# Performance work log

Hardware: AMD Instinct MI355X
Metric: run time of the kernel (lower is better)

Reference implementation:

```python
import jax, jax.numpy as jnp
import numpy as np

N1, N2, E, D, DOUT = 20000, 20000, 1000000, 64, 64


def setup_inputs() -> dict:
    key = jax.random.key(0)
    ks = jax.random.split(key, 10)
    node1 = jax.random.normal(ks[0], (N1, D), jnp.float32)
    node2 = jax.random.normal(ks[1], (N2, D), jnp.float32)
    seg_i1 = jax.random.randint(ks[2], (E,), 0, N1, dtype=jnp.int32)
    idx_j1 = jax.random.randint(ks[3], (E,), 0, 64, dtype=jnp.int32)
    seg_i2 = jax.random.randint(ks[4], (E,), 0, N2, dtype=jnp.int32)
    idx_j2 = jax.random.randint(ks[5], (E,), 0, 64, dtype=jnp.int32)
    xav = float(np.sqrt(2.0 / (D + D)))  # xavier_normal for square proj
    Wk = jax.random.normal(ks[6], (D, D), jnp.float32) * xav
    Wv = jax.random.normal(ks[7], (D, D), jnp.float32) * xav
    Wo = jax.random.normal(ks[8], (D, DOUT), jnp.float32) * float(np.sqrt(1.0 / D))
    bo = jnp.zeros((DOUT,), jnp.float32)
    return {"node1": node1, "seg_i1": seg_i1, "idx_j1": idx_j1,
            "node2": node2, "seg_i2": seg_i2, "idx_j2": idx_j2,
            "Wk": Wk, "Wv": Wv, "Wo": Wo, "bo": bo}


def _segment_softmax(logit, seg, n_seg, temperature):
    # faithful to torch segment_softmax: max is detached; idx_j dense-buffer
    # trick is equivalent to a true segment max for unique (seg, idx) pairs
    m = jax.lax.stop_gradient(jax.ops.segment_max(logit, seg, num_segments=n_seg))
    e = jnp.exp((logit - m[seg]) / temperature)
    s = jax.ops.segment_sum(e, seg, num_segments=n_seg)
    return e / (s[seg] + 1e-8)


def reference(node1, seg_i1, idx_j1, node2, seg_i2, idx_j2, Wk, Wv, Wo, bo):
    d_h = node1.shape[1]
    n_seg1, n_seg2 = node1.shape[0], node2.shape[0]
    temperature = float(np.sqrt(d_h))

    node1_ctr = (node1 @ Wk)[seg_i1]   # [E, d_h]
    node2_ctr = (node2 @ Wk)[seg_i2]
    node1_nbr = (node2 @ Wv)[seg_i2]
    node2_nbr = (node1 @ Wv)[seg_i1]

    translation = jnp.sum(node1_ctr * node2_ctr, axis=1)  # [E]

    node1_edge = _segment_softmax(translation, seg_i1, n_seg1, temperature)
    node2_edge = _segment_softmax(translation, seg_i2, n_seg2, temperature)

    msg1 = jax.ops.segment_sum(node1_edge[:, None] * node1_nbr, seg_i1, num_segments=n_seg1)
    msg2 = jax.ops.segment_sum(node2_edge[:, None] * node2_nbr, seg_i2, num_segments=n_seg2)

    msg1 = jax.nn.leaky_relu(msg1 @ Wo + bo, negative_slope=0.01)
    msg2 = jax.nn.leaky_relu(msg2 @ Wo + bo, negative_slope=0.01)
    return msg1, msg2, node1_edge[:, None], node2_edge[:, None]
```

## Files before the change

kernel.cpp:

```cpp
#include <hip/hip_runtime.h>
#include <math.h>

#define BSH 7
#define BSZ (1 << BSH)
#define MAXNB 256
#define PT_TILE 4096

typedef __attribute__((ext_vector_type(4))) float f32x4;
typedef __attribute__((ext_vector_type(8))) short bf16x8;

__device__ __forceinline__ float readlane_f(float v, int l) {
    return __uint_as_float((unsigned)__builtin_amdgcn_readlane((int)__float_as_uint(v), l));
}
__device__ __forceinline__ unsigned short f2b(float f) {
    unsigned u = __float_as_uint(f);
    return (unsigned short)((u + 0x7FFFu + ((u >> 16) & 1u)) >> 16);
}
__device__ __forceinline__ float blo(unsigned u) { return __uint_as_float(u << 16); }
__device__ __forceinline__ float bhi(unsigned u) { return __uint_as_float(u & 0xFFFF0000u); }

__global__ void proj_kernel(const float* __restrict__ X1, int n1,
                            const float* __restrict__ X2, int n2,
                            const float* __restrict__ Wk,
                            const float* __restrict__ Wv,
                            unsigned short* __restrict__ K1, unsigned short* __restrict__ V1,
                            unsigned short* __restrict__ K2, unsigned short* __restrict__ V2,
                            int* bcnt1, int* bcnt2, int nb1, int nb2) {
    __shared__ float sWk[64 * 64];
    __shared__ float sWv[64 * 64];
    int tid = threadIdx.x;
    if (blockIdx.x == 0) {
        for (int i = tid; i < nb1; i += blockDim.x) bcnt1[i] = 0;
        for (int i = tid; i < nb2; i += blockDim.x) bcnt2[i] = 0;
    }
    for (int i = tid; i < 1024; i += blockDim.x) {
        ((float4*)sWk)[i] = ((const float4*)Wk)[i];
        ((float4*)sWv)[i] = ((const float4*)Wv)[i];
    }
    __syncthreads();
    int wave = tid >> 6, lane = tid & 63;
    int wpb = blockDim.x >> 6;
    int total = n1 + n2;
    for (int idx = blockIdx.x * wpb + wave; idx < total; idx += gridDim.x * wpb) {
        const float* X; unsigned short* K; unsigned short* V; long r;
        if (idx < n1) { X = X1; K = K1; V = V1; r = idx; }
        else { X = X2; K = K2; V = V2; r = idx - n1; }
        float x = X[r * 64 + lane];
        float ak = 0.f, av = 0.f;
#pragma unroll
        for (int k = 0; k < 64; ++k) {
            float xv = __shfl(x, k);
            ak = fmaf(xv, sWk[k * 64 + lane], ak);
            av = fmaf(xv, sWv[k * 64 + lane], av);
        }
        K[r * 64 + lane] = f2b(ak);
        V[r * 64 + lane] = f2b(av);
    }
}

__global__ void logit_kernel(const unsigned short* __restrict__ K1,
                             const unsigned short* __restrict__ K2,
                             const int* __restrict__ seg1, const int* __restrict__ seg2,
                             float* __restrict__ trans, int E) {
    int tid = blockIdx.x * blockDim.x + threadIdx.x;
    int e = tid >> 3, g = tid & 7;
    if (e >= E) return;
    int i1 = seg1[e], i2 = seg2[e];
    uint4 a = *(const uint4*)(K1 + (long)i1 * 64 + g * 8);
    uint4 b = *(const uint4*)(K2 + (long)i2 * 64 + g * 8);
    float d = blo(a.x) * blo(b.x);
    d = fmaf(bhi(a.x), bhi(b.x), d);
    d = fmaf(blo(a.y), blo(b.y), d);
    d = fmaf(bhi(a.y), bhi(b.y), d);
    d = fmaf(blo(a.z), blo(b.z), d);
    d = fmaf(bhi(a.z), bhi(b.z), d);
    d = fmaf(blo(a.w), blo(b.w), d);
    d = fmaf(bhi(a.w), bhi(b.w), d);
    d += __shfl_xor(d, 1);
    d += __shfl_xor(d, 2);
    d += __shfl_xor(d, 4);
    if (g == 0) trans[e] = d;
}

__global__ void bucket_count_kernel(const int* __restrict__ seg1, const int* __restrict__ seg2,
                                    int E, int* bcnt1, int* bcnt2, int nb1, int nb2) {
    __shared__ int c1[MAXNB], c2[MAXNB];
    int tid = threadIdx.x;
    for (int i = tid; i < MAXNB; i += blockDim.x) { c1[i] = 0; c2[i] = 0; }
    __syncthreads();
    for (int i = blockIdx.x * blockDim.x + tid; i < E; i += gridDim.x * blockDim.x) {
        atomicAdd(&c1[seg1[i] >> BSH], 1);
        atomicAdd(&c2[seg2[i] >> BSH], 1);
    }
    __syncthreads();
    for (int i = tid; i < nb1; i += blockDim.x) if (c1[i]) atomicAdd(&bcnt1[i], c1[i]);
    for (int i = tid; i < nb2; i += blockDim.x) if (c2[i]) atomicAdd(&bcnt2[i], c2[i]);
}

__global__ void bucket_scan_kernel(const int* __restrict__ bcnt1, const int* __restrict__ bcnt2,
                                   int* bb1, int* bb2, int* bcur1, int* bcur2,
                                   int nb1, int nb2, int E) {
    __shared__ int tmp[MAXNB];
    int t = threadIdx.x;
    int v1 = (t < nb1) ? bcnt1[t] : 0;
    tmp[t] = v1;
    __syncthreads();
    for (int off = 1; off < MAXNB; off <<= 1) {
        int x = (t >= off) ? tmp[t - off] : 0;
        __syncthreads();
        tmp[t] += x;
        __syncthreads();
    }
    if (t < nb1) { int excl = tmp[t] - v1; bb1[t] = excl; bcur1[t] = excl; }
    if (t == 0) bb1[nb1] = E;
    __syncthreads();
    int v2 = (t < nb2) ? bcnt2[t] : 0;
    tmp[t] = v2;
    __syncthreads();
    for (int off = 1; off < MAXNB; off <<= 1) {
        int x = (t >= off) ? tmp[t - off] : 0;
        __syncthreads();
        tmp[t] += x;
        __syncthreads();
    }
    if (t < nb2) { int excl = tmp[t] - v2; bb2[t] = excl; bcur2[t] = excl; }
    if (t == 0) bb2[nb2] = E;
}

__global__ void partition_kernel(const int* __restrict__ seg1, const int* __restrict__ seg2,
                                 const float* __restrict__ trans, int E,
                                 int* bcur1, int* bcur2,
                                 float2* __restrict__ tmp1, float2* __restrict__ tmp2) {
    __shared__ int c1[MAXNB], c2[MAXNB];
    int tid = threadIdx.x;
    int base = blockIdx.x * PT_TILE;
    int end = base + PT_TILE;
    if (end > E) end = E;
    for (int i = tid; i < MAXNB; i += blockDim.x) { c1[i] = 0; c2[i] = 0; }
    __syncthreads();
    for (int i = base + tid; i < end; i += blockDim.x) {
        atomicAdd(&c1[seg1[i] >> BSH], 1);
        atomicAdd(&c2[seg2[i] >> BSH], 1);
    }
    __syncthreads();
    for (int i = tid; i < MAXNB; i += blockDim.x) {
        int n = c1[i]; c1[i] = n ? atomicAdd(&bcur1[i], n) : 0;
        n = c2[i];     c2[i] = n ? atomicAdd(&bcur2[i], n) : 0;
    }
    __syncthreads();
    for (int i = base + tid; i < end; i += blockDim.x) {
        int s1 = seg1[i], s2 = seg2[i];
        float t = trans[i];
        int p = atomicAdd(&c1[s1 >> BSH], 1);
        tmp1[p] = make_float2(t, __int_as_float(((s1 & (BSZ - 1)) << 25) | s2));
        int q = atomicAdd(&c2[s2 >> BSH], 1);
        tmp2[q] = make_float2(t, __int_as_float(((s2 & (BSZ - 1)) << 25) | s1));
    }
}

__global__ void bin2_kernel(const float2* __restrict__ tmp1, const int* __restrict__ bb1,
                            int n1, int* __restrict__ cur1, int* __restrict__ deg1,
                            float2* __restrict__ csr1,
                            const float2* __restrict__ tmp2, const int* __restrict__ bb2,
                            int n2, int* __restrict__ cur2, int* __restrict__ deg2,
                            float2* __restrict__ csr2, int nb1) {
    __shared__ int cnt[BSZ];
    __shared__ int off[BSZ];
    __shared__ int sc[BSZ];
    int b = blockIdx.x;
    const float2* tmp; const int* bb; int n; int* cur; int* deg; float2* csr;
    if (b < nb1) { tmp = tmp1; bb = bb1; n = n1; cur = cur1; deg = deg1; csr = csr1; }
    else { b -= nb1; tmp = tmp2; bb = bb2; n = n2; cur = cur2; deg = deg2; csr = csr2; }
    int tid = threadIdx.x;
    int node0 = b << BSH;
    int s = bb[b], e_end = bb[b + 1];
    for (int i = tid; i < BSZ; i += blockDim.x) cnt[i] = 0;
    __syncthreads();
    for (int i = s + tid; i < e_end; i += blockDim.x)
        atomicAdd(&cnt[((unsigned)__float_as_int(tmp[i].y)) >> 25], 1);
    __syncthreads();
    if (tid < BSZ) sc[tid] = cnt[tid];
    __syncthreads();
    for (int o = 1; o < BSZ; o <<= 1) {
        int x = (tid >= o && tid < BSZ) ? sc[tid - o] : 0;
        __syncthreads();
        if (tid < BSZ) sc[tid] += x;
        __syncthreads();
    }
    if (tid < BSZ) {
        int excl = sc[tid] - cnt[tid] + s;
        off[tid] = excl;
        int node = node0 + tid;
        if (node < n) { cur[node] = excl; deg[node] = cnt[tid]; }
    }
    __syncthreads();
    for (int i = s + tid; i < e_end; i += blockDim.x) {
        float2 r = tmp[i];
        unsigned pay = (unsigned)__float_as_int(r.y);
        int pos = atomicAdd(&off[pay >> 25], 1);
        csr[pos] = make_float2(r.x, __int_as_float((int)(pay & 0x1FFFFFFu)));
    }
}

__global__ void gather_ms_kernel(int n1, int n2,
                                 const int* __restrict__ cur1, const int* __restrict__ deg1,
                                 const float2* __restrict__ csr1,
                                 const unsigned short* __restrict__ Vb2,
                                 float2* __restrict__ minv1,
                                 const int* __restrict__ cur2, const int* __restrict__ deg2,
                                 const float2* __restrict__ csr2,
                                 const unsigned short* __restrict__ Vb1,
                                 float2* __restrict__ minv2,
                                 unsigned short* __restrict__ msgr,
                                 float invT) {
    int tid = threadIdx.x;
    int wave = tid >> 6, lane = tid & 63;
    int wpb = blockDim.x >> 6;
    int g = lane >> 4, l = lane & 15;
    int total = n1 + n2;
    for (int idx = blockIdx.x * wpb + wave; idx < total; idx += gridDim.x * wpb) {
        const int *cur, *deg; const float2* csr; const unsigned short* V;
        float2* minv; int nd;
        if (idx < n1) {
            cur = cur1; deg = deg1; csr = csr1; V = Vb2; minv = minv1; nd = idx;
        } else {
            cur = cur2; deg = deg2; csr = csr2; V = Vb1; minv = minv2; nd = idx - n1;
        }
        int d = deg[nd];
        int start = cur[nd];
        float4 acc = make_float4(0.f, 0.f, 0.f, 0.f);
        if (d > 0) {
            float t0 = -INFINITY, t1 = -INFINITY, t2 = -INFINITY;
            int j0 = 0, j1 = 0, j2 = 0;
            if (lane < d)       { float2 r = csr[start + lane];       t0 = r.x; j0 = __float_as_int(r.y); }
            if (lane + 64 < d)  { float2 r = csr[start + lane + 64];  t1 = r.x; j1 = __float_as_int(r.y); }
            if (lane + 128 < d) { float2 r = csr[start + lane + 128]; t2 = r.x; j2 = __float_as_int(r.y); }
            float m = fmaxf(fmaxf(t0, t1), t2);
            for (int k = 192 + lane; k < d; k += 64) m = fmaxf(m, csr[start + k].x);
            m = fmaxf(m, __shfl_xor(m, 1));
            m = fmaxf(m, __shfl_xor(m, 2));
            m = fmaxf(m, __shfl_xor(m, 4));
            m = fmaxf(m, __shfl_xor(m, 8));
            m = fmaxf(m, __shfl_xor(m, 16));
            m = fmaxf(m, __shfl_xor(m, 32));
            float p0 = (lane < d)       ? __expf((t0 - m) * invT) : 0.f;
            float p1 = (lane + 64 < d)  ? __expf((t1 - m) * invT) : 0.f;
            float p2 = (lane + 128 < d) ? __expf((t2 - m) * invT) : 0.f;
            float s = p0 + p1 + p2;
            for (int k = 192 + lane; k < d; k += 64) s += __expf((csr[start + k].x - m) * invT);
            s += __shfl_xor(s, 1);
            s += __shfl_xor(s, 2);
            s += __shfl_xor(s, 4);
            s += __shfl_xor(s, 8);
            s += __shfl_xor(s, 16);
            s += __shfl_xor(s, 32);
            float inv = 1.f / (s + 1e-8f);
            if (lane == 0) minv[nd] = make_float2(m, inv);
            unsigned u0 = ((unsigned)f2b(p0 * inv) << 16) | (unsigned)j0;
            unsigned u1 = ((unsigned)f2b(p1 * inv) << 16) | (unsigned)j1;
            unsigned u2 = ((unsigned)f2b(p2 * inv) << 16) | (unsigned)j2;
            int c0 = d < 64 ? d : 64;
#pragma unroll 8
            for (int k = 0; k < c0; k += 4) {
                unsigned u = (unsigned)__shfl((int)u0, k + g);
                float w = bhi(u);
                int j = (int)(u & 0xFFFFu);
                uint2 v = *(const uint2*)(V + (long)j * 64 + l * 4);
                acc.x = fmaf(w, blo(v.x), acc.x);
                acc.y = fmaf(w, bhi(v.x), acc.y);
                acc.z = fmaf(w, blo(v.y), acc.z);
                acc.w = fmaf(w, bhi(v.y), acc.w);
            }
            if (d > 64) {
                int c1 = (d - 64) < 64 ? (d - 64) : 64;
#pragma unroll 8
                for (int k = 0; k < c1; k += 4) {
                    unsigned u = (unsigned)__shfl((int)u1, k + g);
                    float w = bhi(u);
                    int j = (int)(u & 0xFFFFu);
                    uint2 v = *(const uint2*)(V + (long)j * 64 + l * 4);
                    acc.x = fmaf(w, blo(v.x), acc.x);
                    acc.y = fmaf(w, bhi(v.x), acc.y);
                    acc.z = fmaf(w, blo(v.y), acc.z);
                    acc.w = fmaf(w, bhi(v.y), acc.w);
                }
            }
            if (d > 128) {
                int c2 = (d - 128) < 64 ? (d - 128) : 64;
#pragma unroll 8
                for (int k = 0; k < c2; k += 4) {
                    unsigned u = (unsigned)__shfl((int)u2, k + g);
                    float w = bhi(u);
                    int j = (int)(u & 0xFFFFu);
                    uint2 v = *(const uint2*)(V + (long)j * 64 + l * 4);
                    acc.x = fmaf(w, blo(v.x), acc.x);
                    acc.y = fmaf(w, bhi(v.x), acc.y);
                    acc.z = fmaf(w, blo(v.y), acc.z);
                    acc.w = fmaf(w, bhi(v.y), acc.w);
                }
            }
            for (int base = 192; base < d; base += 64) {
                int k = base + lane;
                unsigned ur = 0;
                if (k < d) {
                    float2 r = csr[start + k];
                    float wr = __expf((r.x - m) * invT) * inv;
                    ur = ((unsigned)f2b(wr) << 16) | (unsigned)(__float_as_int(r.y) & 0xFFFF);
                }
                int cc = (d - base) < 64 ? (d - base) : 64;
                for (int k2 = 0; k2 < cc; k2 += 4) {
                    unsigned u = (unsigned)__shfl((int)ur, k2 + g);
                    float w = bhi(u);
                    int j = (int)(u & 0xFFFFu);
                    uint2 v = *(const uint2*)(V + (long)j * 64 + l * 4);
                    acc.x = fmaf(w, blo(v.x), acc.x);
                    acc.y = fmaf(w, bhi(v.x), acc.y);
                    acc.z = fmaf(w, blo(v.y), acc.z);
                    acc.w = fmaf(w, bhi(v.y), acc.w);
                }
            }
            acc.x += __shfl_xor(acc.x, 16); acc.y += __shfl_xor(acc.y, 16);
            acc.z += __shfl_xor(acc.z, 16); acc.w += __shfl_xor(acc.w, 16);
            acc.x += __shfl_xor(acc.x, 32); acc.y += __shfl_xor(acc.y, 32);
            acc.z += __shfl_xor(acc.z, 32); acc.w += __shfl_xor(acc.w, 32);
        }
        if (g == 0) {
            uint2 p;
            p.x = (unsigned)f2b(acc.x) | ((unsigned)f2b(acc.y) << 16);
            p.y = (unsigned)f2b(acc.z) | ((unsigned)f2b(acc.w) << 16);
            *(uint2*)(msgr + (long)idx * 64 + l * 4) = p;
        }
    }
}

__global__ void out_mfma_kernel(const unsigned short* __restrict__ msgr,
                                float* __restrict__ outp,
                                const float* __restrict__ Wo,
                                const float* __restrict__ bo,
                                int total) {
    int lane = threadIdx.x & 63;
    int wave = threadIdx.x >> 6;
    int wpb = blockDim.x >> 6;
    int ntiles = (total + 15) >> 4;
    int tile = blockIdx.x * wpb + wave;
    if (tile >= ntiles) return;
    int r0 = tile << 4;
    int rr = r0 + (lane & 15);
    if (rr > total - 1) rr = total - 1;
    int kg = lane >> 4;
    int k0 = kg * 8;
    int c = lane & 15;
    const unsigned short* pr = msgr + (long)rr * 64;
    bf16x8 a0 = *(const bf16x8*)(pr + k0);
    bf16x8 a1 = *(const bf16x8*)(pr + k0 + 32);
    int orow0 = kg * 4;
#pragma unroll
    for (int n0 = 0; n0 < 64; n0 += 16) {
        bf16x8 b0, b1;
#pragma unroll
        for (int t = 0; t < 8; ++t) {
            b0[t] = (short)f2b(Wo[(k0 + t) * 64 + n0 + c]);
            b1[t] = (short)f2b(Wo[(k0 + 32 + t) * 64 + n0 + c]);
        }
        f32x4 acc = {0.f, 0.f, 0.f, 0.f};
        acc = __builtin_amdgcn_mfma_f32_16x16x32_bf16(a0, b0, acc, 0, 0, 0);
        acc = __builtin_amdgcn_mfma_f32_16x16x32_bf16(a1, b1, acc, 0, 0, 0);
        float bias = bo[n0 + c];
#pragma unroll
        for (int q = 0; q < 4; ++q) {
            int r = r0 + orow0 + q;
            if (r < total) {
                float o = acc[q] + bias;
                o = (o >= 0.f) ? o : 0.01f * o;
                outp[(long)r * 64 + n0 + c] = o;
            }
        }
    }
}

__global__ void edge_w_kernel(const float* __restrict__ trans,
                              const int* __restrict__ seg1, const int* __restrict__ seg2,
                              const float2* __restrict__ minv1, const float2* __restrict__ minv2,
                              float* __restrict__ e1, float* __restrict__ e2,
                              int E, float invT) {
    int e = blockIdx.x * blockDim.x + threadIdx.x;
    if (e >= E) return;
    float t = trans[e];
    float2 a = minv1[seg1[e]];
    float2 b = minv2[seg2[e]];
    e1[e] = __expf((t - a.x) * invT) * a.y;
    e2[e] = __expf((t - b.x) * invT) * b.y;
}

__global__ void proj1_kernel(const float* __restrict__ X, int N,
                             const float* __restrict__ Wk,
                             const float* __restrict__ Wv,
                             float* __restrict__ K, float* __restrict__ V) {
    __shared__ float sWk[64 * 64];
    __shared__ float sWv[64 * 64];
    int tid = threadIdx.x;
    for (int i = tid; i < 4096; i += blockDim.x) { sWk[i] = Wk[i]; sWv[i] = Wv[i]; }
    __syncthreads();
    int wave = tid >> 6, lane = tid & 63;
    int wpb = blockDim.x >> 6;
    for (int n = blockIdx.x * wpb + wave; n < N; n += gridDim.x * wpb) {
        float x = X[n * 64 + lane];
        float ak = 0.f, av = 0.f;
#pragma unroll
        for (int k = 0; k < 64; ++k) {
            float xv = __shfl(x, k);
            ak = fmaf(xv, sWk[k * 64 + lane], ak);
            av = fmaf(xv, sWv[k * 64 + lane], av);
        }
        K[n * 64 + lane] = ak;
        V[n * 64 + lane] = av;
    }
}
__global__ void logit1_kernel(const float* __restrict__ K1, const float* __restrict__ K2,
                              const int* __restrict__ seg1, const int* __restrict__ seg2,
                              float* __restrict__ trans, int E) {
    int tid = blockIdx.x * blockDim.x + threadIdx.x;
    int e = tid >> 4, g = tid & 15;
    if (e >= E) return;
    int i1 = seg1[e], i2 = seg2[e];
    float4 a = ((const float4*)(K1 + (long)i1 * 64))[g];
    float4 b = ((const float4*)(K2 + (long)i2 * 64))[g];
    float d = a.x * b.x + a.y * b.y + a.z * b.z + a.w * b.w;
    d += __shfl_xor(d, 1);
    d += __shfl_xor(d, 2);
    d += __shfl_xor(d, 4);
    d += __shfl_xor(d, 8);
    if (g == 0) trans[e] = d;
}
__global__ void zero_deg_kernel(int* d1, int* d2, int n1, int n2) {
    int i = blockIdx.x * blockDim.x + threadIdx.x;
    if (i < n1) d1[i] = 0;
    if (i < n2) d2[i] = 0;
}
__global__ void hist_kernel(const int* __restrict__ seg1, const int* __restrict__ seg2,
                            int* deg1, int* deg2, int E) {
    int e = blockIdx.x * blockDim.x + threadIdx.x;
    if (e >= E) return;
    atomicAdd(&deg1[seg1[e]], 1);
    atomicAdd(&deg2[seg2[e]], 1);
}
__global__ void scan2_kernel(const int* __restrict__ d1, int* __restrict__ c1, int n1,
                             const int* __restrict__ d2, int* __restrict__ c2, int n2) {
    const int* deg = blockIdx.x ? d2 : d1;
    int* cur = blockIdx.x ? c2 : c1;
    int n = blockIdx.x ? n2 : n1;
    __shared__ int tmp[1024];
    __shared__ int s_carry;
    int t = threadIdx.x;
    if (t == 0) s_carry = 0;
    __syncthreads();
    for (int base = 0; base < n; base += 1024) {
        int idx = base + t;
        int v = (idx < n) ? deg[idx] : 0;
        tmp[t] = v;
        __syncthreads();
        for (int off = 1; off < 1024; off <<= 1) {
            int x = (t >= off) ? tmp[t - off] : 0;
            __syncthreads();
            tmp[t] += x;
            __syncthreads();
        }
        int excl = tmp[t] - v + s_carry;
        if (idx < n) cur[idx] = excl;
        __syncthreads();
        if (t == 0) s_carry += tmp[1023];
        __syncthreads();
    }
}
__global__ void bin_kernel(const int* __restrict__ seg1, const int* __restrict__ seg2,
                           int* cur1, int* cur2,
                           int* __restrict__ el1, int* __restrict__ el2, int E) {
    int e = blockIdx.x * blockDim.x + threadIdx.x;
    if (e >= E) return;
    int p1 = atomicAdd(&cur1[seg1[e]], 1);
    el1[p1] = e;
    int p2 = atomicAdd(&cur2[seg2[e]], 1);
    el2[p2] = e;
}
__global__ void gather_out_kernel(int N, const int* __restrict__ cur, const int* __restrict__ deg,
                                  const int* __restrict__ el, const float* __restrict__ trans,
                                  const int* __restrict__ segOther, const float* __restrict__ Vother,
                                  float* __restrict__ e_out, float* __restrict__ msg_out,
                                  const float* __restrict__ Wo, const float* __restrict__ bo,
                                  float invT) {
    __shared__ float sW[64 * 64];
    int tid = threadIdx.x;
    for (int i = tid; i < 4096; i += blockDim.x) sW[i] = Wo[i];
    __syncthreads();
    int wave = tid >> 6, lane = tid & 63;
    int wpb = blockDim.x >> 6;
    int node = blockIdx.x * wpb + wave;
    if (node >= N) return;
    int d = deg[node];
    int start = cur[node] - d;
    float acc = 0.f;
    if (d > 0) {
        float m = -INFINITY;
        for (int k = lane; k < d; k += 64) m = fmaxf(m, trans[el[start + k]]);
        m = fmaxf(m, __shfl_xor(m, 1));
        m = fmaxf(m, __shfl_xor(m, 2));
        m = fmaxf(m, __shfl_xor(m, 4));
        m = fmaxf(m, __shfl_xor(m, 8));
        m = fmaxf(m, __shfl_xor(m, 16));
        m = fmaxf(m, __shfl_xor(m, 32));
        float s = 0.f;
        for (int k = lane; k < d; k += 64) s += __expf((trans[el[start + k]] - m) * invT);
        s += __shfl_xor(s, 1);
        s += __shfl_xor(s, 2);
        s += __shfl_xor(s, 4);
        s += __shfl_xor(s, 8);
        s += __shfl_xor(s, 16);
        s += __shfl_xor(s, 32);
        float inv = 1.f / (s + 1e-8f);
        for (int base = 0; base < d; base += 64) {
            int k = base + lane;
            float w = 0.f;
            int j = 0;
            if (k < d) {
                int e = el[start + k];
                w = __expf((trans[e] - m) * invT) * inv;
                e_out[e] = w;
                j = segOther[e];
            }
            int cnt = (d - base < 64) ? (d - base) : 64;
            for (int q = 0; q < cnt; ++q) {
                float wq = __shfl(w, q);
                int jq = __shfl(j, q);
                acc = fmaf(wq, Vother[(long)jq * 64 + lane], acc);
            }
        }
    }
    float o = bo[lane];
#pragma unroll
    for (int k = 0; k < 64; ++k) {
        float xv = __shfl(acc, k);
        o = fmaf(xv, sW[k * 64 + lane], o);
    }
    o = (o >= 0.f) ? o : 0.01f * o;
    msg_out[(long)node * 64 + lane] = o;
}

extern "C" void kernel_launch(void* const* d_in, const int* in_sizes, int n_in,
                              void* d_out, int out_size, void* d_ws, size_t ws_size,
                              hipStream_t stream) {
    const float* node1 = (const float*)d_in[0];
    const int* seg1 = (const int*)d_in[1];
    const float* node2 = (const float*)d_in[3];
    const int* seg2 = (const int*)d_in[4];
    const float* Wk = (const float*)d_in[6];
    const float* Wv = (const float*)d_in[7];
    const float* Wo = (const float*)d_in[8];
    const float* bo = (const float*)d_in[9];

    int n1 = in_sizes[0] / 64;
    int n2 = in_sizes[3] / 64;
    int E = in_sizes[1];

    float* out = (float*)d_out;
    float* msg1 = out;
    float* msg2 = msg1 + (long)n1 * 64;
    float* e1 = msg2 + (long)n2 * 64;
    float* e2 = e1 + E;

    const float invT = 1.0f / sqrtf(64.0f);
    int nb1 = (n1 + BSZ - 1) >> BSH;
    int nb2 = (n2 + BSZ - 1) >> BSH;
    long Epad = (E + 1) & ~1L;

    float* ws = (float*)d_ws;
    float2* csr1 = (float2*)ws;
    float2* csr2 = csr1 + E;
    float2* tmp1 = csr2 + E;
    float2* tmp2 = tmp1 + E;
    float* trans = (float*)(tmp2 + E);
    float2* minv1 = (float2*)(trans + Epad);
    float2* minv2 = minv1 + n1;
    unsigned short* Kb1 = (unsigned short*)(minv2 + n2);
    unsigned short* Kb2 = Kb1 + (long)n1 * 64;
    unsigned short* Vb1 = Kb2 + (long)n2 * 64;
    unsigned short* Vb2 = Vb1 + (long)n1 * 64;
    unsigned short* msgr = Vb2 + (long)n2 * 64;
    int* deg1 = (int*)(msgr + (long)(n1 + n2) * 64);
    int* deg2 = deg1 + n1;
    int* cur1 = deg2 + n2;
    int* cur2 = cur1 + n1;
    int* bb1 = cur2 + n2;
    int* bb2 = bb1 + nb1 + 1;
    int* bcur1 = bb2 + nb2 + 1;
    int* bcur2 = bcur1 + nb1;
    int* bcnt1 = bcur2 + nb2;
    int* bcnt2 = bcnt1 + nb1;
    long fp_words = 8L * E + Epad + 2L * (n1 + n2)
                  + 64L * (n1 + n2)
                  + 32L * (n1 + n2)
                  + 2L * (n1 + n2)
                  + 3L * (nb1 + nb2) + 2;
    bool fast = (E <= (1 << 20)) && (nb1 <= MAXNB) && (nb2 <= MAXNB)
             && (n1 < 65536) && (n2 < 65536) && (n1 + n2 > 0)
             && ((size_t)fp_words * 4 <= ws_size);

    if (fast) {
        int total = n1 + n2;
        int gp = (total + 3) / 4;
        if (gp > 1024) gp = 1024;
        int gg = (total + 3) / 4;
        if (gg > 2048) gg = 2048;
        proj_kernel<<<gp, 256, 0, stream>>>(node1, n1, node2, n2, Wk, Wv,
                                            Kb1, Vb1, Kb2, Vb2,
                                            bcnt1, bcnt2, nb1, nb2);
        {
            long threads = (long)E * 8;
            int blocks = (int)((threads + 255) / 256);
            logit_kernel<<<blocks, 256, 0, stream>>>(Kb1, Kb2, seg1, seg2, trans, E);
        }
        bucket_count_kernel<<<512, 256, 0, stream>>>(seg1, seg2, E, bcnt1, bcnt2, nb1, nb2);
        bucket_scan_kernel<<<1, MAXNB, 0, stream>>>(bcnt1, bcnt2, bb1, bb2, bcur1, bcur2,
                                                    nb1, nb2, E);
        partition_kernel<<<(E + PT_TILE - 1) / PT_TILE, 256, 0, stream>>>(
            seg1, seg2, trans, E, bcur1, bcur2, tmp1, tmp2);
        bin2_kernel<<<nb1 + nb2, 256, 0, stream>>>(tmp1, bb1, n1, cur1, deg1, csr1,
                                                   tmp2, bb2, n2, cur2, deg2, csr2, nb1);
        gather_ms_kernel<<<gg, 256, 0, stream>>>(
            n1, n2, cur1, deg1, csr1, Vb2, minv1,
            cur2, deg2, csr2, Vb1, minv2, msgr, invT);
        {
            int ntiles = (total + 15) / 16;
            int blocks = (ntiles + 3) / 4;
            out_mfma_kernel<<<blocks, 256, 0, stream>>>(msgr, msg1, Wo, bo, total);
        }
        edge_w_kernel<<<(E + 255) / 256, 256, 0, stream>>>(
            trans, seg1, seg2, minv1, minv2, e1, e2, E, invT);
    } else {
        float* K1f = ws;
        float* V1f = K1f + (long)n1 * 64;
        float* K2f = V1f + (long)n1 * 64;
        float* V2f = K2f + (long)n2 * 64;
        float* transf = V2f + (long)n2 * 64;
        int* deg1f = (int*)(transf + E);
        int* deg2f = deg1f + n1;
        int* cur1f = deg2f + n2;
        int* cur2f = cur1f + n1;
        int* el1 = (int*)K1f;
        int* el2 = (int*)K2f;

        proj1_kernel<<<(n1 + 3) / 4, 256, 0, stream>>>(node1, n1, Wk, Wv, K1f, V1f);
        proj1_kernel<<<(n2 + 3) / 4, 256, 0, stream>>>(node2, n2, Wk, Wv, K2f, V2f);
        {
            long threads = (long)E * 16;
            int blocks = (int)((threads + 255) / 256);
            logit1_kernel<<<blocks, 256, 0, stream>>>(K1f, K2f, seg1, seg2, transf, E);
        }
        zero_deg_kernel<<<((n1 > n2 ? n1 : n2) + 255) / 256, 256, 0, stream>>>(deg1f, deg2f, n1, n2);
        hist_kernel<<<(E + 255) / 256, 256, 0, stream>>>(seg1, seg2, deg1f, deg2f, E);
        scan2_kernel<<<2, 1024, 0, stream>>>(deg1f, cur1f, n1, deg2f, cur2f, n2);
        bin_kernel<<<(E + 255) / 256, 256, 0, stream>>>(seg1, seg2, cur1f, cur2f, el1, el2, E);

        gather_out_kernel<<<(n1 + 3) / 4, 256, 0, stream>>>(
            n1, cur1f, deg1f, el1, transf, seg2, V2f, e1, msg1, Wo, bo, invT);
        gather_out_kernel<<<(n2 + 3) / 4, 256, 0, stream>>>(
            n2, cur2f, deg2f, el2, transf, seg1, V1f, e2, msg2, Wo, bo, invT);
    }
}
```

Before: 198.8 us.

## Run K/V projection on MFMA with pre-transposed bf16 weights

Replaces the per-row shuffle-and-FMA projection kernel with a 16-row-tile MFMA kernel that converts inputs to bf16 and multiplies them against bf16 weights. A new single-block prep kernel transposes and converts Wk, Wv and Wo once into workspace and also zeroes the bucket counters. The output MFMA kernel now loads the pre-transposed Wo as vector loads instead of doing strided scalar loads with per-element conversion. This adds one extra serial launch, and rounding the node features to bf16 before the projection slightly changes numerics.

```diff
diff --git a/kernel.cpp b/kernel.cpp
--- a/kernel.cpp
+++ b/kernel.cpp
@@ -9,9 +9,6 @@
 typedef __attribute__((ext_vector_type(4))) float f32x4;
 typedef __attribute__((ext_vector_type(8))) short bf16x8;
 
-__device__ __forceinline__ float readlane_f(float v, int l) {
-    return __uint_as_float((unsigned)__builtin_amdgcn_readlane((int)__float_as_uint(v), l));
-}
 __device__ __forceinline__ unsigned short f2b(float f) {
     unsigned u = __float_as_uint(f);
     return (unsigned short)((u + 0x7FFFu + ((u >> 16) & 1u)) >> 16);
@@ -19,42 +16,76 @@
 __device__ __forceinline__ float blo(unsigned u) { return __uint_as_float(u << 16); }
 __device__ __forceinline__ float bhi(unsigned u) { return __uint_as_float(u & 0xFFFF0000u); }
 
-__global__ void proj_kernel(const float* __restrict__ X1, int n1,
-                            const float* __restrict__ X2, int n2,
-                            const float* __restrict__ Wk,
-                            const float* __restrict__ Wv,
-                            unsigned short* __restrict__ K1, unsigned short* __restrict__ V1,
-                            unsigned short* __restrict__ K2, unsigned short* __restrict__ V2,
+__global__ void prep_kernel(const float* __restrict__ Wk, const float* __restrict__ Wv,
+                            const float* __restrict__ Wo,
+                            unsigned short* __restrict__ WkT, unsigned short* __restrict__ WvT,
+                            unsigned short* __restrict__ WoT,
                             int* bcnt1, int* bcnt2, int nb1, int nb2) {
-    __shared__ float sWk[64 * 64];
-    __shared__ float sWv[64 * 64];
     int tid = threadIdx.x;
-    if (blockIdx.x == 0) {
-        for (int i = tid; i < nb1; i += blockDim.x) bcnt1[i] = 0;
-        for (int i = tid; i < nb2; i += blockDim.x) bcnt2[i] = 0;
-    }
-    for (int i = tid; i < 1024; i += blockDim.x) {
-        ((float4*)sWk)[i] = ((const float4*)Wk)[i];
-        ((float4*)sWv)[i] = ((const float4*)Wv)[i];
-    }
-    __syncthreads();
-    int wave = tid >> 6, lane = tid & 63;
+    for (int i = tid; i < nb1; i += blockDim.x) bcnt1[i] = 0;
+    for (int i = tid; i < nb2; i += blockDim.x) bcnt2[i] = 0;
+    for (int i = tid; i < 4096; i += blockDim.x) {
+        int k = i >> 6, c = i & 63;
+        WkT[c * 64 + k] = f2b(Wk[i]);
+        WvT[c * 64 + k] = f2b(Wv[i]);
+        WoT[c * 64 + k] = f2b(Wo[i]);
+    }
+}
+
+__global__ void proj_mfma_kernel(const float* __restrict__ X1, int n1,
+                                 const float* __restrict__ X2, int n2,
+                                 const unsigned short* __restrict__ WkT,
+                                 const unsigned short* __restrict__ WvT,
+                                 unsigned short* __restrict__ Kall,
+                                 unsigned short* __restrict__ Vall) {
+    int lane = threadIdx.x & 63;
+    int wave = threadIdx.x >> 6;
     int wpb = blockDim.x >> 6;
     int total = n1 + n2;
-    for (int idx = blockIdx.x * wpb + wave; idx < total; idx += gridDim.x * wpb) {
-        const float* X; unsigned short* K; unsigned short* V; long r;
-        if (idx < n1) { X = X1; K = K1; V = V1; r = idx; }
-        else { X = X2; K = K2; V = V2; r = idx - n1; }
-        float x = X[r * 64 + lane];
-        float ak = 0.f, av = 0.f;
+    int ntiles = (total + 15) >> 4;
+    int tile = blockIdx.x * wpb + wave;
+    if (tile >= ntiles) return;
+    int r0 = tile << 4;
+    int rr = r0 + (lane & 15);
+    if (rr > total - 1) rr = total - 1;
+    int kg = lane >> 4;
+    int k0 = kg * 8;
+    int c = lane & 15;
+    const float* xp = (rr < n1) ? (X1 + (long)rr * 64) : (X2 + (long)(rr - n1) * 64);
+    float4 xa = *(const float4*)(xp + k0);
+    float4 xb = *(const float4*)(xp + k0 + 4);
+    float4 xc = *(const float4*)(xp + k0 + 32);
+    float4 xd = *(const float4*)(xp + k0 + 36);
+    bf16x8 a0, a1;
+    a0[0] = (short)f2b(xa.x); a0[1] = (short)f2b(xa.y);
+    a0[2] = (short)f2b(xa.z); a0[3] = (short)f2b(xa.w);
+    a0[4] = (short)f2b(xb.x); a0[5] = (short)f2b(xb.y);
+    a0[6] = (short)f2b(xb.z); a0[7] = (short)f2b(xb.w);
+    a1[0] = (short)f2b(xc.x); a1[1] = (short)f2b(xc.y);
+    a1[2] = (short)f2b(xc.z); a1[3] = (short)f2b(xc.w);
+    a1[4] = (short)f2b(xd.x); a1[5] = (short)f2b(xd.y);
+    a1[6] = (short)f2b(xd.z); a1[7] = (short)f2b(xd.w);
+    int orow0 = kg * 4;
 #pragma unroll
-        for (int k = 0; k < 64; ++k) {
-            float xv = __shfl(x, k);
-            ak = fmaf(xv, sWk[k * 64 + lane], ak);
-            av = fmaf(xv, sWv[k * 64 + lane], av);
-        }
-        K[r * 64 + lane] = f2b(ak);
-        V[r * 64 + lane] = f2b(av);
+    for (int n0 = 0; n0 < 64; n0 += 16) {
+        bf16x8 bk0 = *(const bf16x8*)(WkT + (n0 + c) * 64 + k0);
+        bf16x8 bk1 = *(const bf16x8*)(WkT + (n0 + c) * 64 + k0 + 32);
+        bf16x8 bv0 = *(const bf16x8*)(WvT + (n0 + c) * 64 + k0);
+        bf16x8 bv1 = *(const bf16x8*)(WvT + (n0 + c) * 64 + k0 + 32);
+        f32x4 aK = {0.f, 0.f, 0.f, 0.f};
+        f32x4 aV = {0.f, 0.f, 0.f, 0.f};
+        aK = __builtin_amdgcn_mfma_f32_16x16x32_bf16(a0, bk0, aK, 0, 0, 0);
+        aK = __builtin_amdgcn_mfma_f32_16x16x32_bf16(a1, bk1, aK, 0, 0, 0);
+        aV = __builtin_amdgcn_mfma_f32_16x16x32_bf16(a0, bv0, aV, 0, 0, 0);
+        aV = __builtin_amdgcn_mfma_f32_16x16x32_bf16(a1, bv1, aV, 0, 0, 0);
+#pragma unroll
+        for (int q = 0; q < 4; ++q) {
+            int r = r0 + orow0 + q;
+            if (r < total) {
+                Kall[(long)r * 64 + n0 + c] = f2b(aK[q]);
+                Vall[(long)r * 64 + n0 + c] = f2b(aV[q]);
+            }
+        }
     }
 }
 
@@ -335,7 +366,7 @@
 
 __global__ void out_mfma_kernel(const unsigned short* __restrict__ msgr,
                                 float* __restrict__ outp,
-                                const float* __restrict__ Wo,
+                                const unsigned short* __restrict__ WoT,
                                 const float* __restrict__ bo,
                                 int total) {
     int lane = threadIdx.x & 63;
@@ -356,12 +387,8 @@
     int orow0 = kg * 4;
 #pragma unroll
     for (int n0 = 0; n0 < 64; n0 += 16) {
-        bf16x8 b0, b1;
-#pragma unroll
-        for (int t = 0; t < 8; ++t) {
-            b0[t] = (short)f2b(Wo[(k0 + t) * 64 + n0 + c]);
-            b1[t] = (short)f2b(Wo[(k0 + 32 + t) * 64 + n0 + c]);
-        }
+        bf16x8 b0 = *(const bf16x8*)(WoT + (n0 + c) * 64 + k0);
+        bf16x8 b1 = *(const bf16x8*)(WoT + (n0 + c) * 64 + k0 + 32);
         f32x4 acc = {0.f, 0.f, 0.f, 0.f};
         acc = __builtin_amdgcn_mfma_f32_16x16x32_bf16(a0, b0, acc, 0, 0, 0);
         acc = __builtin_amdgcn_mfma_f32_16x16x32_bf16(a1, b1, acc, 0, 0, 0);
@@ -573,7 +600,10 @@
     long Epad = (E + 1) & ~1L;
 
     float* ws = (float*)d_ws;
-    float2* csr1 = (float2*)ws;
+    unsigned short* WkT = (unsigned short*)ws;
+    unsigned short* WvT = WkT + 4096;
+    unsigned short* WoT = WvT + 4096;
+    float2* csr1 = (float2*)(ws + 6144);
     float2* csr2 = csr1 + E;
     float2* tmp1 = csr2 + E;
     float2* tmp2 = tmp1 + E;
@@ -595,7 +625,7 @@
     int* bcur2 = bcur1 + nb1;
     int* bcnt1 = bcur2 + nb2;
     int* bcnt2 = bcnt1 + nb1;
-    long fp_words = 8L * E + Epad + 2L * (n1 + n2)
+    long fp_words = 6144 + 8L * E + Epad + 2L * (n1 + n2)
                   + 64L * (n1 + n2)
                   + 32L * (n1 + n2)
                   + 2L * (n1 + n2)
@@ -606,13 +636,13 @@
 
     if (fast) {
         int total = n1 + n2;
-        int gp = (total + 3) / 4;
-        if (gp > 1024) gp = 1024;
+        int ntiles = (total + 15) / 16;
         int gg = (total + 3) / 4;
         if (gg > 2048) gg = 2048;
-        proj_kernel<<<gp, 256, 0, stream>>>(node1, n1, node2, n2, Wk, Wv,
-                                            Kb1, Vb1, Kb2, Vb2,
-                                            bcnt1, bcnt2, nb1, nb2);
+        prep_kernel<<<1, 256, 0, stream>>>(Wk, Wv, Wo, WkT, WvT, WoT,
+                                           bcnt1, bcnt2, nb1, nb2);
+        proj_mfma_kernel<<<(ntiles + 3) / 4, 256, 0, stream>>>(
+            node1, n1, node2, n2, WkT, WvT, Kb1, Vb1);
         {
             long threads = (long)E * 8;
             int blocks = (int)((threads + 255) / 256);
@@ -629,9 +659,8 @@
             n1, n2, cur1, deg1, csr1, Vb2, minv1,
             cur2, deg2, csr2, Vb1, minv2, msgr, invT);
         {
-            int ntiles = (total + 15) / 16;
             int blocks = (ntiles + 3) / 4;
-            out_mfma_kernel<<<blocks, 256, 0, stream>>>(msgr, msg1, Wo, bo, total);
+            out_mfma_kernel<<<blocks, 256, 0, stream>>>(msgr, msg1, WoT, bo, total);
         }
         edge_w_kernel<<<(E + 255) / 256, 256, 0, stream>>>(
             trans, seg1, seg2, minv1, minv2, e1, e2, E, invT);
```

After: 178.0 us. -10.5%, faster.
